# Kernel tuning notes

Measured on AMD Instinct MI355X. Metric: run time of the kernel, lower is better.

Reference implementation:

```python
import jax, jax.numpy as jnp
import numpy as np

B, N, D = 8, 1024, 256
H, U = 8, 64  # num_heads, units per head


def setup_inputs() -> dict:
    key = jax.random.key(0)
    ks = jax.random.split(key, 8)
    X = jax.random.normal(ks[0], (B, N, D), dtype=jnp.float32)
    A = (jax.random.uniform(ks[1], (B, N, N)) < 0.1).astype(jnp.float32)
    A = jnp.maximum(A, jnp.eye(N, dtype=jnp.float32)[None])
    s = 1.0 / np.sqrt(D)
    kernel = jax.random.normal(ks[2], (D, H * U), dtype=jnp.float32) * s
    kernel_residual = jax.random.normal(ks[3], (D, H * U), dtype=jnp.float32) * s
    su = 1.0 / np.sqrt(U)
    attn_kernel_self = jax.random.normal(ks[4], (H, U, 1), dtype=jnp.float32) * su
    attn_kernel_neighs = jax.random.normal(ks[5], (H, U, 1), dtype=jnp.float32) * su
    bias = jnp.zeros((H * U,), dtype=jnp.float32)
    return {
        "X": X, "A": A,
        "kernel": kernel, "kernel_residual": kernel_residual,
        "attn_kernel_self": attn_kernel_self,
        "attn_kernel_neighs": attn_kernel_neighs,
        "bias": bias,
    }


def reference(X, A, kernel, kernel_residual, attn_kernel_self, attn_kernel_neighs, bias):
    # feature projections: [B,N,H*U]
    features = X @ kernel
    features_residual = X @ kernel_residual
    f = features.reshape(B, N, H, U)  # bnhu
    # additive attention logits per head
    attn_self = jnp.einsum('bnhu,hu->bnh', f, attn_kernel_self[..., 0])
    attn_neigh = jnp.einsum('bnhu,hu->bnh', f, attn_kernel_neighs[..., 0])
    dense = attn_self[:, :, None, :] + attn_neigh[:, None, :, :]  # b n k h
    dense = jax.nn.leaky_relu(dense, negative_slope=0.2)
    # mask non-edges, softmax over neighbor axis k
    dense = dense + (-1e10) * (1.0 - A)[..., None]
    attn_coef = jax.nn.softmax(dense, axis=2)
    # (dropout is identity in inference mode)
    node_features = jnp.einsum('bnkh,bkhu->bnhu', attn_coef, f)
    node_features = node_features.reshape(B, N, H * U) + features_residual + bias
    # head_reduction == 'concat' -> keep [B,N,H*U]
    return jax.nn.relu(node_features)
```

## Files before the change

kernel.cpp:

```cpp
#include <hip/hip_runtime.h>
#include <stdint.h>


typedef __attribute__((ext_vector_type(8))) short short8;
typedef __attribute__((ext_vector_type(4))) float f32x4;

__device__ __forceinline__ unsigned short f32_to_bf16(float f) {
    unsigned int u = __float_as_uint(f);
    u = (u + 0x7fffu + ((u >> 16) & 1u)) >> 16;
    return (unsigned short)u;
}
__device__ __forceinline__ float bf16_to_f32(unsigned short s) {
    return __uint_as_float(((unsigned int)s) << 16);
}
__device__ __forceinline__ void load_lds16(const unsigned short* g, unsigned short* l) {
    __builtin_amdgcn_global_load_lds(
        (const __attribute__((address_space(1))) unsigned int*)g,
        (__attribute__((address_space(3))) unsigned int*)l, 16, 0, 0);
}

__global__ __launch_bounds__(256) void pack_a(const float* __restrict__ X,
                                              unsigned short* __restrict__ Abig) {
    const int idx = blockIdx.x * 256 + threadIdx.x;
    const int m  = idx >> 6;
    const int kg = (idx & 63) << 2;
    float4 x = *(const float4*)&X[m * 256 + kg];
    const float xs[4] = {x.x, x.y, x.z, x.w};
    union { unsigned short u[4]; uint64_t q; } hq, lq;
    #pragma unroll
    for (int i = 0; i < 4; i++) {
        unsigned short h = f32_to_bf16(xs[i]);
        hq.u[i] = h;
        lq.u[i] = f32_to_bf16(xs[i] - bf16_to_f32(h));
    }
    unsigned short* r = Abig + (size_t)m * 768;
    *(uint64_t*)(r + kg)       = hq.q;
    *(uint64_t*)(r + 256 + kg) = hq.q;
    *(uint64_t*)(r + 512 + kg) = lq.q;
}

__global__ __launch_bounds__(256) void pack_b(const float* __restrict__ Wk,
                                              const float* __restrict__ Wr,
                                              unsigned short* __restrict__ Bpack) {
    const int idx = blockIdx.x * 256 + threadIdx.x;
    const int n = idx / 768;
    const int k = idx - n * 768;
    const float* __restrict__ W = (n < 512) ? Wk : Wr;
    const int nc = n & 511;
    const float w = W[(k & 255) * 512 + nc];
    unsigned short h = f32_to_bf16(w);
    unsigned short o = (k >= 256 && k < 512) ? f32_to_bf16(w - bf16_to_f32(h)) : h;
    Bpack[idx] = o;
}

__global__ __launch_bounds__(512) void attn_ck(const float* __restrict__ kernel,
                                               const float* __restrict__ aks,
                                               const float* __restrict__ akn,
                                               float* __restrict__ ck) {
    const int d = blockIdx.x, j = threadIdx.x;
    const float kv = kernel[d * 512 + j];
    float a = kv * aks[j];
    float b = kv * akn[j];
    #pragma unroll
    for (int m = 32; m; m >>= 1) { a += __shfl_xor(a, m, 64); b += __shfl_xor(b, m, 64); }
    const int lane = j & 63, h = j >> 6;
    if (lane == 0) {
        ck[d * 16 + h]     = a * 1.4426950408889634f;
        ck[d * 16 + 8 + h] = b * 1.4426950408889634f;
    }
}

__global__ __launch_bounds__(256) void attn_sa(const float* __restrict__ X,
                                               const float* __restrict__ ck,
                                               float* __restrict__ as_g,
                                               float* __restrict__ an_Tg) {
    __shared__ __align__(16) float Xs[16][260];
    __shared__ __align__(16) float ckL[4096];
    const int t = threadIdx.x, row0 = blockIdx.x * 16;
    #pragma unroll
    for (int i = 0; i < 4; i++) {
        const int q = t + i * 256;
        const int r = q >> 6, c4 = (q & 63) * 4;
        *(float4*)&Xs[r][c4] = *(const float4*)&X[(size_t)(row0 + r) * 256 + c4];
        *(float4*)&ckL[q * 4] = *(const float4*)&ck[q * 4];
    }
    __syncthreads();
    const int r = t >> 4, o = t & 15;
    float acc = 0.f;
    #pragma unroll 4
    for (int d = 0; d < 256; d++) acc = fmaf(Xs[r][d], ckL[d * 16 + o], acc);
    const int grow = row0 + r;
    if (o < 8)
        as_g[(size_t)grow * 8 + o] = acc;
    else
        an_Tg[((size_t)(grow >> 10) * 8 + (o - 8)) * 1024 + (grow & 1023)] = acc;
}

#define GK 768
__global__ __launch_bounds__(256) void gemm_bf16(const unsigned short* __restrict__ Ab,
                                                 const unsigned short* __restrict__ Bp,
                                                 unsigned short* __restrict__ featT,
                                                 float* __restrict__ outr) {
    __shared__ __align__(16) unsigned short As[128 * 32];
    __shared__ __align__(16) unsigned short Bs[128 * 32];
    const int tid = threadIdx.x;
    const int lane = tid & 63, wave = tid >> 6;
    const int wr = wave >> 1, wc = wave & 1;
    const int m0 = blockIdx.x * 128, n0 = blockIdx.y * 128;
    const int l15 = lane & 15, lhi = lane >> 4;

    f32x4 acc[4][4] = {};

    for (int k0 = 0; k0 < GK; k0 += 32) {
        #pragma unroll
        for (int i = 0; i < 2; i++) {
            const int s = tid + i * 256;
            const int row = s >> 2, kc = (s & 3) * 8;
            load_lds16(Ab + (size_t)(m0 + row) * GK + k0 + kc, &As[s * 8]);
            load_lds16(Bp + (size_t)(n0 + row) * GK + k0 + kc, &Bs[s * 8]);
        }
        asm volatile("s_waitcnt vmcnt(0)" ::: "memory");
        __syncthreads();
        short8 a[4], b[4];
        #pragma unroll
        for (int mi = 0; mi < 4; mi++)
            a[mi] = *(const short8*)&As[(wr * 64 + mi * 16 + l15) * 32 + lhi * 8];
        #pragma unroll
        for (int ni = 0; ni < 4; ni++)
            b[ni] = *(const short8*)&Bs[(wc * 64 + ni * 16 + l15) * 32 + lhi * 8];
        #pragma unroll
        for (int mi = 0; mi < 4; mi++)
            #pragma unroll
            for (int ni = 0; ni < 4; ni++)
                acc[mi][ni] = __builtin_amdgcn_mfma_f32_16x16x32_bf16(a[mi], b[ni], acc[mi][ni], 0, 0, 0);
        __syncthreads();
    }

    if (n0 < 512) {
        #pragma unroll
        for (int mi = 0; mi < 4; mi++)
            #pragma unroll
            for (int ni = 0; ni < 4; ni++) {
                const int col = n0 + wc * 64 + ni * 16 + l15;
                const int rbase = m0 + wr * 64 + mi * 16 + lhi * 4;
                const int bb = rbase >> 10, nl = rbase & 1023;
                union { unsigned short u[4]; uint64_t q; } pk;
                #pragma unroll
                for (int r = 0; r < 4; r++) pk.u[r] = f32_to_bf16(acc[mi][ni][r]);
                *(uint64_t*)&featT[(size_t)bb * 524288 + (size_t)col * 1024 + nl] = pk.q;
            }
    } else {
        #pragma unroll
        for (int mi = 0; mi < 4; mi++)
            #pragma unroll
            for (int ni = 0; ni < 4; ni++) {
                const int col = (n0 - 512) + wc * 64 + ni * 16 + l15;
                const int rbase = m0 + wr * 64 + mi * 16 + lhi * 4;
                #pragma unroll
                for (int r = 0; r < 4; r++)
                    outr[(size_t)(rbase + r) * 512 + col] = acc[mi][ni][r];
            }
    }
}

__global__ __launch_bounds__(1024) void gat_mfma2(
    const float* __restrict__ A, const unsigned short* __restrict__ featT,
    const float* __restrict__ as_g, const float* __restrict__ an_Tg,
    const float* __restrict__ bias, float* __restrict__ out) {
    __shared__ float an_T[8192];
    __shared__ unsigned int maskA[32][33];

    const int blk = blockIdx.x;
    const int b  = blk & 7;
    const int n0 = (blk >> 3) * 32;
    const int t = threadIdx.x;
    const int w16 = t >> 6;
    const int h = w16 & 7, half = w16 >> 3;
    const int lane = t & 63, l15 = lane & 15, lhi = lane >> 4;

    {
        const float* __restrict__ src = an_Tg + (size_t)b * 8192;
        *(float4*)&an_T[t * 8]     = *(const float4*)&src[t * 8];
        *(float4*)&an_T[t * 8 + 4] = *(const float4*)&src[t * 8 + 4];
    }
    {
        const int row = t >> 5, wd = t & 31;
        const float* __restrict__ ap = A + ((size_t)(b << 10) + n0 + row) * 1024 + wd * 32;
        unsigned int m = 0;
        #pragma unroll
        for (int i = 0; i < 8; i++) {
            float4 v = *(const float4*)&ap[i * 4];
            if (v.x > 0.5f) m |= 1u << (i * 4 + 0);
            if (v.y > 0.5f) m |= 1u << (i * 4 + 1);
            if (v.z > 0.5f) m |= 1u << (i * 4 + 2);
            if (v.w > 0.5f) m |= 1u << (i * 4 + 3);
        }
        maskA[row][wd] = m;
    }

    const int arow = half * 16 + l15;
    const float as_r = as_g[((size_t)(b << 10) + n0 + arow) * 8 + h];

    short8 ones;
    #pragma unroll
    for (int i = 0; i < 8; i++) ones[i] = (short)0x3F80;

    f32x4 acc[4] = {};
    f32x4 accs = {};
    const unsigned short* __restrict__ fT =
        featT + (size_t)b * 524288 + (size_t)(h * 64) * 1024;

    __syncthreads();

    for (int k0 = 0; k0 < 1024; k0 += 32) {
        const unsigned int m = maskA[arow][k0 >> 5];
        const float* __restrict__ anp = &an_T[h * 1024 + k0 + lhi * 8];
        float4 an0 = *(const float4*)&anp[0];
        float4 an1 = *(const float4*)&anp[4];
        const float av[8] = {an0.x, an0.y, an0.z, an0.w, an1.x, an1.y, an1.z, an1.w};

        union { short8 s8; unsigned int u32[4]; } pa;
        #pragma unroll
        for (int q = 0; q < 4; q++) {
            float pv[2];
            #pragma unroll
            for (int d = 0; d < 2; d++) {
                const int j = q * 2 + d;
                float x = as_r + av[j];
                x = fmaxf(x, 0.2f * x);
                const float e = __builtin_amdgcn_exp2f(x);
                pv[d] = (m & (1u << (lhi * 8 + j))) ? e : 0.f;
            }
            unsigned int pk;
            asm("v_cvt_pk_bf16_f32 %0, %1, %2" : "=v"(pk) : "v"(pv[0]), "v"(pv[1]));
            pa.u32[q] = pk;
        }
        short8 bf[4];
        #pragma unroll
        for (int ni = 0; ni < 4; ni++)
            bf[ni] = *(const short8*)&fT[(size_t)(ni * 16 + l15) * 1024 + k0 + lhi * 8];
        #pragma unroll
        for (int ni = 0; ni < 4; ni++)
            acc[ni] = __builtin_amdgcn_mfma_f32_16x16x32_bf16(pa.s8, bf[ni], acc[ni], 0, 0, 0);
        accs = __builtin_amdgcn_mfma_f32_16x16x32_bf16(pa.s8, ones, accs, 0, 0, 0);
    }

    #pragma unroll
    for (int r = 0; r < 4; r++) {
        const int row_l = half * 16 + lhi * 4 + r;
        const float iv = 1.0f / accs[r];
        const size_t rb = ((size_t)(b << 10) + n0 + row_l) * 512 + h * 64;
        #pragma unroll
        for (int ni = 0; ni < 4; ni++) {
            const int col = ni * 16 + l15;
            const float v = fmaf(acc[ni][r], iv, out[rb + col] + bias[h * 64 + col]);
            out[rb + col] = fmaxf(v, 0.f);
        }
    }
}

extern "C" void kernel_launch(void* const* d_in, const int* in_sizes, int n_in,
                              void* d_out, int out_size, void* d_ws, size_t ws_size,
                              hipStream_t stream) {
    const float* X    = (const float*)d_in[0];
    const float* A    = (const float*)d_in[1];
    const float* Wk   = (const float*)d_in[2];
    const float* Wr   = (const float*)d_in[3];
    const float* aks  = (const float*)d_in[4];
    const float* akn  = (const float*)d_in[5];
    const float* bias = (const float*)d_in[6];
    float* out = (float*)d_out;

    unsigned short* featT = (unsigned short*)d_ws;
    float* as_g  = (float*)(featT + (size_t)8 * 512 * 1024);
    float* an_Tg = as_g + 65536;
    float* ck    = an_Tg + 65536;
    unsigned short* Abig  = (unsigned short*)(ck + 4096);
    unsigned short* Bpack = Abig + (size_t)8192 * 768;

    pack_a<<<2048, 256, 0, stream>>>(X, Abig);
    pack_b<<<3072, 256, 0, stream>>>(Wk, Wr, Bpack);
    attn_ck<<<256, 512, 0, stream>>>(Wk, aks, akn, ck);
    attn_sa<<<512, 256, 0, stream>>>(X, ck, as_g, an_Tg);
    gemm_bf16<<<dim3(64, 8), 256, 0, stream>>>(Abig, Bpack, featT, out);
    gat_mfma2<<<256, 1024, 0, stream>>>(A, featT, as_g, an_Tg, bias, out);
}
```

Before: 193.8 us.

## Factor exp of leaky-relu logits into precomputed exponent products, halve GAT tile

Uses exp2(leaky(a+b)) = max(exp2(a)exp2(b), exp2(0.2a)exp2(0.2b)) so the attention kernel computes the exponentials once per node in attn_sa. The neighbor exponents are stored as packed bf16 pairs, and the inner loop does two multiplies and a max instead of an add, leaky-relu and exp. The GAT kernel also moves to 16-row tiles with 512 threads and 512 blocks to raise occupancy. The risks are bf16 precision loss on the neighbor exponents, possible overflow or underflow without max subtraction, and each block re-reading featT for half as many rows.

```diff
diff --git a/kernel.cpp b/kernel.cpp
--- a/kernel.cpp
+++ b/kernel.cpp
@@ -72,8 +72,8 @@
 
 __global__ __launch_bounds__(256) void attn_sa(const float* __restrict__ X,
                                                const float* __restrict__ ck,
-                                               float* __restrict__ as_g,
-                                               float* __restrict__ an_Tg) {
+                                               float2* __restrict__ as2,
+                                               unsigned int* __restrict__ anE) {
     __shared__ __align__(16) float Xs[16][260];
     __shared__ __align__(16) float ckL[4096];
     const int t = threadIdx.x, row0 = blockIdx.x * 16;
@@ -90,10 +90,15 @@
     #pragma unroll 4
     for (int d = 0; d < 256; d++) acc = fmaf(Xs[r][d], ckL[d * 16 + o], acc);
     const int grow = row0 + r;
-    if (o < 8)
-        as_g[(size_t)grow * 8 + o] = acc;
-    else
-        an_Tg[((size_t)(grow >> 10) * 8 + (o - 8)) * 1024 + (grow & 1023)] = acc;
+    const float e1 = __builtin_amdgcn_exp2f(acc);
+    const float e2 = __builtin_amdgcn_exp2f(0.2f * acc);
+    if (o < 8) {
+        as2[(size_t)grow * 8 + o] = make_float2(e1, e2);
+    } else {
+        unsigned int pk;
+        asm("v_cvt_pk_bf16_f32 %0, %1, %2" : "=v"(pk) : "v"(e1), "v"(e2));
+        anE[((size_t)(grow >> 10) * 8 + (o - 8)) * 1024 + (grow & 1023)] = pk;
+    }
 }
 
 #define GK 768
@@ -163,25 +168,27 @@
     }
 }
 
-__global__ __launch_bounds__(1024) void gat_mfma2(
+__global__ __launch_bounds__(512, 8) void gat_mfma3(
     const float* __restrict__ A, const unsigned short* __restrict__ featT,
-    const float* __restrict__ as_g, const float* __restrict__ an_Tg,
+    const float2* __restrict__ as2, const unsigned int* __restrict__ anE,
     const float* __restrict__ bias, float* __restrict__ out) {
-    __shared__ float an_T[8192];
-    __shared__ unsigned int maskA[32][33];
+    __shared__ unsigned int EanL[8192];
+    __shared__ unsigned int maskA[16][33];
 
     const int blk = blockIdx.x;
     const int b  = blk & 7;
-    const int n0 = (blk >> 3) * 32;
+    const int n0 = (blk >> 3) * 16;
     const int t = threadIdx.x;
-    const int w16 = t >> 6;
-    const int h = w16 & 7, half = w16 >> 3;
+    const int h = t >> 6;
     const int lane = t & 63, l15 = lane & 15, lhi = lane >> 4;
 
     {
-        const float* __restrict__ src = an_Tg + (size_t)b * 8192;
-        *(float4*)&an_T[t * 8]     = *(const float4*)&src[t * 8];
-        *(float4*)&an_T[t * 8 + 4] = *(const float4*)&src[t * 8 + 4];
+        const unsigned int* __restrict__ src = anE + (size_t)b * 8192;
+        #pragma unroll
+        for (int i = 0; i < 4; i++) {
+            const int idx = t + i * 512;
+            *(uint4*)&EanL[idx * 4] = *(const uint4*)&src[idx * 4];
+        }
     }
     {
         const int row = t >> 5, wd = t & 31;
@@ -198,8 +205,8 @@
         maskA[row][wd] = m;
     }
 
-    const int arow = half * 16 + l15;
-    const float as_r = as_g[((size_t)(b << 10) + n0 + arow) * 8 + h];
+    const float2 asv = as2[((size_t)(b << 10) + n0 + l15) * 8 + h];
+    const float ea1 = asv.x, ea2 = asv.y;
 
     short8 ones;
     #pragma unroll
@@ -213,11 +220,11 @@
     __syncthreads();
 
     for (int k0 = 0; k0 < 1024; k0 += 32) {
-        const unsigned int m = maskA[arow][k0 >> 5];
-        const float* __restrict__ anp = &an_T[h * 1024 + k0 + lhi * 8];
-        float4 an0 = *(const float4*)&anp[0];
-        float4 an1 = *(const float4*)&anp[4];
-        const float av[8] = {an0.x, an0.y, an0.z, an0.w, an1.x, an1.y, an1.z, an1.w};
+        const unsigned int mm = maskA[l15][k0 >> 5] >> (lhi * 8);
+        const unsigned int* __restrict__ ep = &EanL[h * 1024 + k0 + lhi * 8];
+        uint4 e0 = *(const uint4*)&ep[0];
+        uint4 e1 = *(const uint4*)&ep[4];
+        const unsigned int ev[8] = {e0.x, e0.y, e0.z, e0.w, e1.x, e1.y, e1.z, e1.w};
 
         union { short8 s8; unsigned int u32[4]; } pa;
         #pragma unroll
@@ -226,10 +233,11 @@
             #pragma unroll
             for (int d = 0; d < 2; d++) {
                 const int j = q * 2 + d;
-                float x = as_r + av[j];
-                x = fmaxf(x, 0.2f * x);
-                const float e = __builtin_amdgcn_exp2f(x);
-                pv[d] = (m & (1u << (lhi * 8 + j))) ? e : 0.f;
+                const unsigned int u = ev[j];
+                const float p1 = ea1 * __uint_as_float(u << 16);
+                const float p2 = ea2 * __uint_as_float(u & 0xFFFF0000u);
+                const float p = fmaxf(p1, p2);
+                pv[d] = (mm & (1u << j)) ? p : 0.f;
             }
             unsigned int pk;
             asm("v_cvt_pk_bf16_f32 %0, %1, %2" : "=v"(pk) : "v"(pv[0]), "v"(pv[1]));
@@ -247,7 +255,7 @@
 
     #pragma unroll
     for (int r = 0; r < 4; r++) {
-        const int row_l = half * 16 + lhi * 4 + r;
+        const int row_l = lhi * 4 + r;
         const float iv = 1.0f / accs[r];
         const size_t rb = ((size_t)(b << 10) + n0 + row_l) * 512 + h * 64;
         #pragma unroll
@@ -272,16 +280,16 @@
     float* out = (float*)d_out;
 
     unsigned short* featT = (unsigned short*)d_ws;
-    float* as_g  = (float*)(featT + (size_t)8 * 512 * 1024);
-    float* an_Tg = as_g + 65536;
-    float* ck    = an_Tg + 65536;
+    float2* as2 = (float2*)(featT + (size_t)8 * 512 * 1024);
+    unsigned int* anE = (unsigned int*)(as2 + (size_t)8192 * 8);
+    float* ck   = (float*)(anE + 65536);
     unsigned short* Abig  = (unsigned short*)(ck + 4096);
     unsigned short* Bpack = Abig + (size_t)8192 * 768;
 
     pack_a<<<2048, 256, 0, stream>>>(X, Abig);
     pack_b<<<3072, 256, 0, stream>>>(Wk, Wr, Bpack);
     attn_ck<<<256, 512, 0, stream>>>(Wk, aks, akn, ck);
-    attn_sa<<<512, 256, 0, stream>>>(X, ck, as_g, an_Tg);
+    attn_sa<<<512, 256, 0, stream>>>(X, ck, as2, anE);
     gemm_bf16<<<dim3(64, 8), 256, 0, stream>>>(Abig, Bpack, featT, out);
-    gat_mfma2<<<256, 1024, 0, stream>>>(A, featT, as_g, an_Tg, bias, out);
-}
+    gat_mfma3<<<512, 512, 0, stream>>>(A, featT, as2, anE, bias, out);
+}
```

Measured after the change: 195.1 us. No clear change (+0.7%).
